# Performance work log

Measured on AMD Instinct MI355X. Metric: run time of the kernel, lower is better.

## Reference

```python
import jax, jax.numpy as jnp
import numpy as np
import math

N_NODES = 100000
N_EDGES = 1600000
IN_CH = 6
HID = 64
OUT_CH = 3


def _lin_init(key, out_c, in_c):
    # torch Linear default: U(-1/sqrt(in_c), 1/sqrt(in_c))
    bound = 1.0 / math.sqrt(in_c)
    return jax.random.uniform(key, (out_c, in_c), jnp.float32, -bound, bound)


def setup_inputs() -> dict:
    key = jax.random.key(0)
    ks = jax.random.split(key, 12)
    x = jax.random.normal(ks[0], (N_NODES, IN_CH), jnp.float32)
    edge_index = jax.random.randint(ks[1], (2, N_EDGES), 0, N_NODES, jnp.int32)
    params = {
        'w1_l': _lin_init(ks[2], HID, IN_CH), 'b1': jnp.zeros((HID,), jnp.float32),
        'w1_r': _lin_init(ks[3], HID, IN_CH),
        'w2_l': _lin_init(ks[4], HID, HID), 'b2': jnp.zeros((HID,), jnp.float32),
        'w2_r': _lin_init(ks[5], HID, HID),
        'w3_l': _lin_init(ks[6], HID, HID), 'b3': jnp.zeros((HID,), jnp.float32),
        'w3_r': _lin_init(ks[7], HID, HID),
        'fc_w': _lin_init(ks[8], OUT_CH, HID), 'fc_b': jnp.zeros((OUT_CH,), jnp.float32),
    }
    return {'x': x, 'edge_index': edge_index, **params}


def _sage_conv(x, src, dst, w_l, b, w_r):
    # mean aggregation of source-node features at destination nodes (PyG SAGEConv)
    deg = jax.ops.segment_sum(jnp.ones((src.shape[0],), x.dtype), dst, num_segments=N_NODES)
    agg = jax.ops.segment_sum(x[src], dst, num_segments=N_NODES)  # [N, C]
    agg = agg / jnp.maximum(deg, 1.0)[:, None]
    # lin_l(aggregated neighbors) + lin_r(self); bias lives in lin_l
    return agg @ w_l.T + b + x @ w_r.T


def reference(x, edge_index, w1_l, b1, w1_r, w2_l, b2, w2_r, w3_l, b3, w3_r, fc_w, fc_b):
    src, dst = edge_index[0], edge_index[1]
    h = jax.nn.relu(_sage_conv(x, src, dst, w1_l, b1, w1_r))
    h = jax.nn.relu(_sage_conv(h, src, dst, w2_l, b2, w2_r))
    h = jax.nn.relu(_sage_conv(h, src, dst, w3_l, b3, w3_r))
    return h @ fc_w.T + fc_b
```

## Files before the change

### kernel.cpp

```cpp
#include <hip/hip_runtime.h>
#include <hip/hip_bf16.h>
#include <hip/hip_fp16.h>

#define N_NODES 100000
#define N_EDGES 1600000
#define NB 391
#define CAP 4608
#define CHUNK 8192
#define NTILES 6250

typedef _Float16 f16x8 __attribute__((ext_vector_type(8)));
typedef _Float16 h16x2 __attribute__((ext_vector_type(2)));
typedef float f32x4 __attribute__((ext_vector_type(4)));

__device__ __forceinline__ float bcast_lane(float v, int k) {
    return __int_as_float(__builtin_amdgcn_readlane(__float_as_int(v), k));
}

__device__ __forceinline__ void acc8(float* a, uint4 v, h16x2 Ev, h16x2 Ov) {
    const h16x2* hp = reinterpret_cast<const h16x2*>(&v);
    a[0] = __builtin_amdgcn_fdot2(hp[0], Ev, a[0], false);
    a[1] = __builtin_amdgcn_fdot2(hp[0], Ov, a[1], false);
    a[2] = __builtin_amdgcn_fdot2(hp[1], Ev, a[2], false);
    a[3] = __builtin_amdgcn_fdot2(hp[1], Ov, a[3], false);
    a[4] = __builtin_amdgcn_fdot2(hp[2], Ev, a[4], false);
    a[5] = __builtin_amdgcn_fdot2(hp[2], Ov, a[5], false);
    a[6] = __builtin_amdgcn_fdot2(hp[3], Ev, a[6], false);
    a[7] = __builtin_amdgcn_fdot2(hp[3], Ov, a[7], false);
}


__global__ void __launch_bounds__(1024) binfill_kernel(
        const int* __restrict__ src, const int* __restrict__ dst,
        int* __restrict__ bincur, unsigned* __restrict__ binned, int e) {
    __shared__ int hcount[NB];
    __shared__ int hloc[NB];
    __shared__ int hbase[NB];
    __shared__ unsigned stage[CHUNK];
    constexpr int Q = CHUNK / 1024;

    int tid = threadIdx.x;
    int base0 = blockIdx.x * CHUNK;

    for (int i = tid; i < NB; i += 1024) hcount[i] = 0;
    __syncthreads();

    int bq[Q]; int rq[Q]; unsigned pq[Q];
    #pragma unroll
    for (int q = 0; q < Q; ++q) {
        int i = base0 + q * 1024 + tid;
        bq[q] = -1;
        if (i < e) {
            int s = src[i], d = dst[i];
            int b = d >> 8;
            bq[q] = b;
            rq[q] = atomicAdd(&hcount[b], 1);
            pq[q] = ((unsigned)s << 8) | (unsigned)(d & 255);
        }
    }
    __syncthreads();

    if (tid < NB) hbase[tid] = atomicAdd(&bincur[tid], hcount[tid]);

    if (tid < 64) {
        int run = 0;
        for (int seg = 0; seg < NB; seg += 64) {
            int idx = seg + tid;
            int d0 = (idx < NB) ? hcount[idx] : 0;
            int v = d0;
            #pragma unroll
            for (int off = 1; off < 64; off <<= 1) {
                int t = __shfl_up(v, off);
                if (tid >= off) v += t;
            }
            if (idx < NB) hloc[idx] = run + v - d0;
            run += __shfl(v, 63);
        }
    }
    __syncthreads();

    #pragma unroll
    for (int q = 0; q < Q; ++q)
        if (bq[q] >= 0) stage[hloc[bq[q]] + rq[q]] = pq[q];
    __syncthreads();

    int w = tid >> 6, lane = tid & 63;
    for (int b = w; b < NB; b += 16) {
        int len = hcount[b];
        int gb0 = hbase[b];
        int lim = min(len, CAP - gb0);
        int lo = hloc[b];
        unsigned* gp = binned + (long long)b * CAP + gb0;
        for (int j = lane; j < lim; j += 64) gp[j] = stage[lo + j];
    }
}


__global__ void binscan_kernel(const int* __restrict__ bincur,
                               int* __restrict__ binbase, int* __restrict__ row_off) {
    int lane = threadIdx.x;
    int run = 0;
    for (int seg = 0; seg < NB; seg += 64) {
        int idx = seg + lane;
        int d = (idx < NB) ? bincur[idx] : 0;
        int v = d;
        #pragma unroll
        for (int off = 1; off < 64; off <<= 1) {
            int t = __shfl_up(v, off);
            if (lane >= off) v += t;
        }
        if (idx < NB) binbase[idx] = run + v - d;
        run += __shfl(v, 63);
    }
    if (lane == 0) row_off[N_NODES] = run;
}


__global__ void __launch_bounds__(512) csrfinal_kernel(
        const unsigned* __restrict__ binned, const int* __restrict__ bincur,
        const int* __restrict__ binbase,
        int* __restrict__ row_off, int* __restrict__ src_sorted) {
    __shared__ int cnt[256];
    __shared__ int wsum[4];
    __shared__ unsigned stage[CAP];
    int b = blockIdx.x, tid = threadIdx.x;
    long long boff = (long long)b * CAP;
    int total = min(bincur[b], CAP);
    int base = binbase[b];

    if (tid < 256) cnt[tid] = 0;
    __syncthreads();
    for (int j = tid; j < total; j += 512) atomicAdd(&cnt[binned[boff + j] & 255u], 1);
    __syncthreads();

    int d = 0, v = 0;
    if (tid < 256) {
        int lane = tid & 63;
        d = cnt[tid];
        v = d;
        #pragma unroll
        for (int off = 1; off < 64; off <<= 1) {
            int t = __shfl_up(v, off);
            if (lane >= off) v += t;
        }
        if (lane == 63) wsum[tid >> 6] = v;
    }
    __syncthreads();
    int excl = 0;
    if (tid < 256) {
        int w = tid >> 6;
        int woff = 0;
        for (int ww = 0; ww < w; ++ww) woff += wsum[ww];
        excl = woff + v - d;
        int node = b * 256 + tid;
        if (node < N_NODES) row_off[node] = base + excl;
    }
    __syncthreads();
    if (tid < 256) cnt[tid] = excl;
    __syncthreads();

    for (int j = tid; j < total; j += 512) {
        unsigned p = binned[boff + j];
        int pos = atomicAdd(&cnt[p & 255u], 1);
        stage[pos] = p >> 8;
    }
    __syncthreads();
    for (int j = tid; j < total; j += 512) src_sorted[base + j] = (int)stage[j];
}


__global__ void wprep_kernel(const float* __restrict__ w_l,
                             const float* __restrict__ w_r,
                             __half* __restrict__ frags) {
    int l = threadIdx.x;
    int col = l & 15, kg = l >> 4;
    #pragma unroll
    for (int f = 0; f < 16; ++f) {
        int mat = f >> 3, kb = (f >> 2) & 1, nt = f & 3;
        const float* W = mat ? w_r : w_l;
        const float* p = W + (nt * 16 + col) * 64 + kb * 32 + kg * 8;
        __half2 hh[4];
        #pragma unroll
        for (int i = 0; i < 4; ++i) hh[i] = __floats2half2_rn(p[2*i], p[2*i+1]);
        *reinterpret_cast<uint4*>(frags + ((size_t)f * 64 + l) * 8) =
            *reinterpret_cast<const uint4*>(hh);
    }
}


template <bool LAST>
__global__ void __launch_bounds__(256) fusedL_kernel(
        const __half* __restrict__ xg,
        const int* __restrict__ row_off, const int* __restrict__ src_sorted,
        const __half* __restrict__ wfrags, const float* __restrict__ bvec,
        const float* __restrict__ fc_w, const float* __restrict__ fc_b,
        __half* __restrict__ hout16, float* __restrict__ out, int ntiles) {
    __shared__ f16x8 sfr[16 * 64];
    int tid = threadIdx.x, lane = tid & 63;

    {
        const uint4* g = reinterpret_cast<const uint4*>(wfrags);
        uint4* s = reinterpret_cast<uint4*>(sfr);
        #pragma unroll
        for (int i = 0; i < 4; ++i) s[tid + i * 256] = g[tid + i * 256];
    }
    __syncthreads();

    int gw = (blockIdx.x * blockDim.x + tid) >> 6;
    int nw = (gridDim.x * blockDim.x) >> 6;
    int nd = lane & 15;
    int sl = lane >> 4;

    const h16x2 Ev = {(_Float16)1.0f, (_Float16)0.0f};
    const h16x2 Ov = {(_Float16)0.0f, (_Float16)1.0f};

    float bias_v[4];
    #pragma unroll
    for (int nt = 0; nt < 4; ++nt) bias_v[nt] = bvec[nt * 16 + nd];
    float fcv0[4], fcv1[4], fcv2[4], fcb0 = 0.f, fcb1 = 0.f, fcb2 = 0.f;
    if (LAST) {
        #pragma unroll
        for (int nt = 0; nt < 4; ++nt) {
            fcv0[nt] = fc_w[0 * 64 + nt * 16 + nd];
            fcv1[nt] = fc_w[1 * 64 + nt * 16 + nd];
            fcv2[nt] = fc_w[2 * 64 + nt * 16 + nd];
        }
        fcb0 = fc_b[0]; fcb1 = fc_b[1]; fcb2 = fc_b[2];
    }

    for (int tile = gw; tile < ntiles; tile += nw) {
        int node = tile * 16 + nd;
        int start = row_off[node], end = row_off[node + 1];
        int deg = end - start;

        float acc[16];
        #pragma unroll
        for (int i = 0; i < 16; ++i) acc[i] = 0.f;

        const int* sp = src_sorted + start;
        int j = 0;
        for (; j + 4 <= deg; j += 4) {
            int s0 = sp[j], s1 = sp[j + 1], s2 = sp[j + 2], s3 = sp[j + 3];
            const __half* p0 = xg + (size_t)s0 * 64 + (sl << 3);
            const __half* p1 = xg + (size_t)s1 * 64 + (sl << 3);
            const __half* p2 = xg + (size_t)s2 * 64 + (sl << 3);
            const __half* p3 = xg + (size_t)s3 * 64 + (sl << 3);
            uint4 va0 = *reinterpret_cast<const uint4*>(p0);
            uint4 va1 = *reinterpret_cast<const uint4*>(p0 + 32);
            uint4 vb0 = *reinterpret_cast<const uint4*>(p1);
            uint4 vb1 = *reinterpret_cast<const uint4*>(p1 + 32);
            uint4 vc0 = *reinterpret_cast<const uint4*>(p2);
            uint4 vc1 = *reinterpret_cast<const uint4*>(p2 + 32);
            uint4 vd0 = *reinterpret_cast<const uint4*>(p3);
            uint4 vd1 = *reinterpret_cast<const uint4*>(p3 + 32);
            acc8(acc,     va0, Ev, Ov);  acc8(acc + 8, va1, Ev, Ov);
            acc8(acc,     vb0, Ev, Ov);  acc8(acc + 8, vb1, Ev, Ov);
            acc8(acc,     vc0, Ev, Ov);  acc8(acc + 8, vc1, Ev, Ov);
            acc8(acc,     vd0, Ev, Ov);  acc8(acc + 8, vd1, Ev, Ov);
        }
        for (; j < deg; ++j) {
            int s0 = sp[j];
            const __half* p0 = xg + (size_t)s0 * 64 + (sl << 3);
            uint4 va0 = *reinterpret_cast<const uint4*>(p0);
            uint4 va1 = *reinterpret_cast<const uint4*>(p0 + 32);
            acc8(acc,     va0, Ev, Ov);
            acc8(acc + 8, va1, Ev, Ov);
        }

        float rs = 1.0f / (float)max(deg, 1);
        union { __half2 h2[4]; f16x8 v; } u0, u1;
        #pragma unroll
        for (int i = 0; i < 4; ++i) {
            u0.h2[i] = __floats2half2_rn(acc[2*i] * rs,     acc[2*i+1] * rs);
            u1.h2[i] = __floats2half2_rn(acc[8+2*i] * rs,   acc[8+2*i+1] * rs);
        }
        f16x8 aa0 = u0.v, aa1 = u1.v;

        const __half* ps = xg + (size_t)node * 64 + (sl << 3);
        f16x8 ah0 = *reinterpret_cast<const f16x8*>(ps);
        f16x8 ah1 = *reinterpret_cast<const f16x8*>(ps + 32);

        float p0a[4] = {0,0,0,0}, p1a[4] = {0,0,0,0}, p2a[4] = {0,0,0,0};
        #pragma unroll
        for (int nt = 0; nt < 4; ++nt) {
            f32x4 acc4 = {0.f, 0.f, 0.f, 0.f};
            acc4 = __builtin_amdgcn_mfma_f32_16x16x32_f16(aa0, sfr[(0  + nt) * 64 + lane], acc4, 0, 0, 0);
            acc4 = __builtin_amdgcn_mfma_f32_16x16x32_f16(aa1, sfr[(4  + nt) * 64 + lane], acc4, 0, 0, 0);
            acc4 = __builtin_amdgcn_mfma_f32_16x16x32_f16(ah0, sfr[(8  + nt) * 64 + lane], acc4, 0, 0, 0);
            acc4 = __builtin_amdgcn_mfma_f32_16x16x32_f16(ah1, sfr[(12 + nt) * 64 + lane], acc4, 0, 0, 0);
            #pragma unroll
            for (int r = 0; r < 4; ++r) {
                float hval = fmaxf(acc4[r] + bias_v[nt], 0.f);
                if (!LAST) {
                    int node_o = tile * 16 + sl * 4 + r;
                    hout16[(size_t)node_o * 64 + nt * 16 + nd] = __float2half(hval);
                } else {
                    p0a[r] = fmaf(hval, fcv0[nt], p0a[r]);
                    p1a[r] = fmaf(hval, fcv1[nt], p1a[r]);
                    p2a[r] = fmaf(hval, fcv2[nt], p2a[r]);
                }
            }
        }
        if (LAST) {
            #pragma unroll
            for (int r = 0; r < 4; ++r) {
                float q0 = p0a[r], q1 = p1a[r], q2 = p2a[r];
                #pragma unroll
                for (int sh = 1; sh <= 8; sh <<= 1) {
                    q0 += __shfl_xor(q0, sh);
                    q1 += __shfl_xor(q1, sh);
                    q2 += __shfl_xor(q2, sh);
                }
                if (nd == 0) {
                    int node_o = tile * 16 + sl * 4 + r;
                    out[(size_t)node_o * 3 + 0] = q0 + fcb0;
                    out[(size_t)node_o * 3 + 1] = q1 + fcb1;
                    out[(size_t)node_o * 3 + 2] = q2 + fcb2;
                }
            }
        }
    }
}

__global__ void __launch_bounds__(256) fused6_kernel(
        const float* __restrict__ xin, const int* __restrict__ row_off,
        const int* __restrict__ src_sorted,
        const float* __restrict__ w_l, const float* __restrict__ bvec,
        const float* __restrict__ w_r,
        __half* __restrict__ hout16, int n) {
    int lane = threadIdx.x & 63;
    int gwid   = (blockIdx.x * blockDim.x + threadIdx.x) >> 6;
    int nwaves = (gridDim.x * blockDim.x) >> 6;
    int e8 = lane >> 3, c = lane & 7;

    float wl[6], wr[6];
    #pragma unroll
    for (int k = 0; k < 6; ++k) { wl[k] = w_l[lane*6 + k]; wr[k] = w_r[lane*6 + k]; }
    float bias = bvec[lane];

    for (int node = gwid; node < n; node += nwaves) {
        int start = row_off[node], end = row_off[node + 1];
        int deg = end - start;
        float acc = 0.f;
        for (int base = start; base < end; base += 64) {
            int cnt = min(64, end - base);
            int sid = (lane < cnt) ? src_sorted[base + lane] : 0;
            for (int jj = 0; jj < cnt; jj += 8) {
                int eidx = jj + e8;
                int s = __shfl(sid, eidx);
                bool valid = (eidx < cnt) && (c < 6);
                float v = valid ? xin[s * 6 + c] : 0.f;
                acc += v;
            }
        }
        #pragma unroll
        for (int sh = 8; sh <= 32; sh <<= 1) acc += __shfl_xor(acc, sh);
        float rs = 1.0f / (float)max(deg, 1);
        float av = acc * rs;
        float hv = (lane < 6) ? xin[node * 6 + lane] : 0.f;

        float o = bias;
        #pragma unroll
        for (int k = 0; k < 6; ++k) {
            o = fmaf(bcast_lane(av, k), wl[k], fmaf(bcast_lane(hv, k), wr[k], o));
        }
        hout16[(size_t)node * 64 + lane] = __float2half(fmaxf(o, 0.f));
    }
}


extern "C" void kernel_launch(void* const* d_in, const int* in_sizes, int n_in,
                              void* d_out, int out_size, void* d_ws, size_t ws_size,
                              hipStream_t stream) {
    const float* x    = (const float*)d_in[0];
    const int*   ei   = (const int*)d_in[1];
    const float* w1_l = (const float*)d_in[2];
    const float* b1   = (const float*)d_in[3];
    const float* w1_r = (const float*)d_in[4];
    const float* w2_l = (const float*)d_in[5];
    const float* b2   = (const float*)d_in[6];
    const float* w2_r = (const float*)d_in[7];
    const float* w3_l = (const float*)d_in[8];
    const float* b3   = (const float*)d_in[9];
    const float* w3_r = (const float*)d_in[10];
    const float* fc_w = (const float*)d_in[11];
    const float* fc_b = (const float*)d_in[12];
    float* out = (float*)d_out;

    const int N = N_NODES;
    const int E = N_EDGES;
    const int* src = ei;
    const int* dst = ei + E;

    size_t off = 0;
    auto alloc = [&](size_t bytes) -> void* {
        void* p = (char*)d_ws + off;
        off += (bytes + 255) & ~size_t(255);
        return p;
    };
    int*      bincur     = (int*)alloc(NB * sizeof(int));
    int*      binbase    = (int*)alloc(NB * sizeof(int));
    unsigned* binned     = (unsigned*)alloc((size_t)NB * CAP * sizeof(unsigned));
    int*      row_off    = (int*)alloc((N + 1) * sizeof(int));
    int*      src_sorted = (int*)alloc((size_t)E * sizeof(int));
    __half*   hA16       = (__half*)alloc((size_t)N * 64 * sizeof(__half));
    __half*   hB16       = (__half*)alloc((size_t)N * 64 * sizeof(__half));
    __half*   wfrags2    = (__half*)alloc(16 * 64 * 8 * sizeof(__half));
    __half*   wfrags3    = (__half*)alloc(16 * 64 * 8 * sizeof(__half));

    hipMemsetAsync(bincur, 0, NB * sizeof(int), stream);

    int nb_fill = (E + CHUNK - 1) / CHUNK;

    binfill_kernel<<<nb_fill, 1024, 0, stream>>>(src, dst, bincur, binned, E);
    binscan_kernel<<<1, 64, 0, stream>>>(bincur, binbase, row_off);
    csrfinal_kernel<<<NB, 512, 0, stream>>>(binned, bincur, binbase, row_off, src_sorted);
    wprep_kernel<<<1, 64, 0, stream>>>(w2_l, w2_r, wfrags2);
    wprep_kernel<<<1, 64, 0, stream>>>(w3_l, w3_r, wfrags3);

    fused6_kernel<<<2048, 256, 0, stream>>>(x, row_off, src_sorted, w1_l, b1, w1_r,
                                            hA16, N);
    fusedL_kernel<false><<<1563, 256, 0, stream>>>(hA16, row_off, src_sorted,
                                                   wfrags2, b2, nullptr, nullptr,
                                                   hB16, nullptr, NTILES);
    fusedL_kernel<true><<<1563, 256, 0, stream>>>(hB16, row_off, src_sorted,
                                                  wfrags3, b3, fc_w, fc_b,
                                                  nullptr, out, NTILES);
}
```

Baseline: 157.3 us.

## Pack layer-1 input to padded fp16 rows and gather one edge per lane

Adds a prep kernel that converts the 6-channel fp32 node features into 16-byte padded fp16 rows. The first-layer kernel then gives each lane one whole neighbour, loaded with a single vector read, instead of 8 edges per pass with one scalar per lane. A full wave reduction then combines the six channel sums. CHUNK in the binning kernel is also halved to launch more blocks. The changes add an extra kernel launch, fp16 rounding of the input features, and more shuffle reductions per node.

```diff
diff --git a/kernel.cpp b/kernel.cpp
--- a/kernel.cpp
+++ b/kernel.cpp
@@ -6,7 +6,7 @@
 #define N_EDGES 1600000
 #define NB 391
 #define CAP 4608
-#define CHUNK 8192
+#define CHUNK 4096
 #define NTILES 6250
 
 typedef _Float16 f16x8 __attribute__((ext_vector_type(8)));
@@ -166,6 +166,20 @@
     }
     __syncthreads();
     for (int j = tid; j < total; j += 512) src_sorted[base + j] = (int)stage[j];
+}
+
+
+__global__ void __launch_bounds__(256) xprep_kernel(
+        const float* __restrict__ x, __half* __restrict__ xg0, int n) {
+    int i = blockIdx.x * blockDim.x + threadIdx.x;
+    if (i >= n) return;
+    const float* p = x + (size_t)i * 6;
+    __half2 o[4];
+    o[0] = __floats2half2_rn(p[0], p[1]);
+    o[1] = __floats2half2_rn(p[2], p[3]);
+    o[2] = __floats2half2_rn(p[4], p[5]);
+    o[3] = __floats2half2_rn(0.f, 0.f);
+    *reinterpret_cast<uint4*>(xg0 + (size_t)i * 8) = *reinterpret_cast<const uint4*>(o);
 }
 
 
@@ -322,8 +336,9 @@
     }
 }
 
+
 __global__ void __launch_bounds__(256) fused6_kernel(
-        const float* __restrict__ xin, const int* __restrict__ row_off,
+        const __half* __restrict__ xg0, const int* __restrict__ row_off,
         const int* __restrict__ src_sorted,
         const float* __restrict__ w_l, const float* __restrict__ bvec,
         const float* __restrict__ w_r,
@@ -331,7 +346,6 @@
     int lane = threadIdx.x & 63;
     int gwid   = (blockIdx.x * blockDim.x + threadIdx.x) >> 6;
     int nwaves = (gridDim.x * blockDim.x) >> 6;
-    int e8 = lane >> 3, c = lane & 7;
 
     float wl[6], wr[6];
     #pragma unroll
@@ -341,29 +355,40 @@
     for (int node = gwid; node < n; node += nwaves) {
         int start = row_off[node], end = row_off[node + 1];
         int deg = end - start;
-        float acc = 0.f;
+
+        float a[6] = {0.f, 0.f, 0.f, 0.f, 0.f, 0.f};
         for (int base = start; base < end; base += 64) {
             int cnt = min(64, end - base);
-            int sid = (lane < cnt) ? src_sorted[base + lane] : 0;
-            for (int jj = 0; jj < cnt; jj += 8) {
-                int eidx = jj + e8;
-                int s = __shfl(sid, eidx);
-                bool valid = (eidx < cnt) && (c < 6);
-                float v = valid ? xin[s * 6 + c] : 0.f;
-                acc += v;
+            if (lane < cnt) {
+                int s = src_sorted[base + lane];
+                uint4 v = *reinterpret_cast<const uint4*>(xg0 + (size_t)s * 8);
+                const __half2* h2 = reinterpret_cast<const __half2*>(&v);
+                float2 f0 = __half22float2(h2[0]);
+                float2 f1 = __half22float2(h2[1]);
+                float2 f2 = __half22float2(h2[2]);
+                a[0] += f0.x; a[1] += f0.y;
+                a[2] += f1.x; a[3] += f1.y;
+                a[4] += f2.x; a[5] += f2.y;
             }
         }
         #pragma unroll
-        for (int sh = 8; sh <= 32; sh <<= 1) acc += __shfl_xor(acc, sh);
+        for (int sh = 1; sh <= 32; sh <<= 1) {
+            #pragma unroll
+            for (int k = 0; k < 6; ++k) a[k] += __shfl_xor(a[k], sh);
+        }
+
+        uint4 vs = *reinterpret_cast<const uint4*>(xg0 + (size_t)node * 8);
+        const __half2* hs = reinterpret_cast<const __half2*>(&vs);
+        float2 s0 = __half22float2(hs[0]);
+        float2 s1 = __half22float2(hs[1]);
+        float2 s2 = __half22float2(hs[2]);
+        float xs[6] = {s0.x, s0.y, s1.x, s1.y, s2.x, s2.y};
+
         float rs = 1.0f / (float)max(deg, 1);
-        float av = acc * rs;
-        float hv = (lane < 6) ? xin[node * 6 + lane] : 0.f;
-
         float o = bias;
         #pragma unroll
-        for (int k = 0; k < 6; ++k) {
-            o = fmaf(bcast_lane(av, k), wl[k], fmaf(bcast_lane(hv, k), wr[k], o));
-        }
+        for (int k = 0; k < 6; ++k)
+            o = fmaf(a[k] * rs, wl[k], fmaf(xs[k], wr[k], o));
         hout16[(size_t)node * 64 + lane] = __float2half(fmaxf(o, 0.f));
     }
 }
@@ -403,6 +428,7 @@
     unsigned* binned     = (unsigned*)alloc((size_t)NB * CAP * sizeof(unsigned));
     int*      row_off    = (int*)alloc((N + 1) * sizeof(int));
     int*      src_sorted = (int*)alloc((size_t)E * sizeof(int));
+    __half*   xg0        = (__half*)alloc((size_t)N * 8 * sizeof(__half));
     __half*   hA16       = (__half*)alloc((size_t)N * 64 * sizeof(__half));
     __half*   hB16       = (__half*)alloc((size_t)N * 64 * sizeof(__half));
     __half*   wfrags2    = (__half*)alloc(16 * 64 * 8 * sizeof(__half));
@@ -415,10 +441,11 @@
     binfill_kernel<<<nb_fill, 1024, 0, stream>>>(src, dst, bincur, binned, E);
     binscan_kernel<<<1, 64, 0, stream>>>(bincur, binbase, row_off);
     csrfinal_kernel<<<NB, 512, 0, stream>>>(binned, bincur, binbase, row_off, src_sorted);
+    xprep_kernel<<<(N + 255) / 256, 256, 0, stream>>>(x, xg0, N);
     wprep_kernel<<<1, 64, 0, stream>>>(w2_l, w2_r, wfrags2);
     wprep_kernel<<<1, 64, 0, stream>>>(w3_l, w3_r, wfrags3);
 
-    fused6_kernel<<<2048, 256, 0, stream>>>(x, row_off, src_sorted, w1_l, b1, w1_r,
+    fused6_kernel<<<2048, 256, 0, stream>>>(xg0, row_off, src_sorted, w1_l, b1, w1_r,
                                             hA16, N);
     fusedL_kernel<false><<<1563, 256, 0, stream>>>(hA16, row_off, src_sorted,
                                                    wfrags2, b2, nullptr, nullptr,
```

Result: slower. 182.3 us (+15.9%).
